# Optimization experiments

Measured on AMD Instinct MI355X. Metric: run time of the kernel, lower is better.

## Reference

```python
import jax, jax.numpy as jnp
import numpy as np

N = 100000       # nodes
E = 3200000      # edges (avg degree 32)
IN_FEATS = 128
HIDDEN = 32
PROP_STEP = 8
USE_RELU = False  # args.relu default


def setup_inputs() -> dict:
    key = jax.random.key(0)
    k1, k2, k3, k4, k5 = jax.random.split(key, 5)
    in_feat = jax.random.normal(k1, (N, IN_FEATS), jnp.float32)
    src = jax.random.randint(k2, (E,), 0, N)
    dst = jax.random.randint(k3, (E,), 0, N)
    # Glorot-ish uniform init like DGL GraphConv weights
    s1 = float(np.sqrt(6.0 / (IN_FEATS + HIDDEN)))
    s2 = float(np.sqrt(6.0 / (HIDDEN + HIDDEN)))
    W1 = jax.random.uniform(k4, (IN_FEATS, HIDDEN), jnp.float32, -s1, s1)
    b1 = jnp.zeros((HIDDEN,), jnp.float32)
    W2 = jax.random.uniform(k5, (HIDDEN, HIDDEN), jnp.float32, -s2, s2)
    b2 = jnp.zeros((HIDDEN,), jnp.float32)
    return {"in_feat": in_feat, "W1": W1, "b1": b1, "W2": W2, "b2": b2,
            "src": src, "dst": dst}


def _graph_conv(x, W, b, src, dst, out_norm, in_norm, weight_first):
    # DGL GraphConv, norm='both':
    #   h = x * out_deg^{-1/2}; (optionally h @ W); SpMM aggregate src->dst;
    #   rst = agg * in_deg^{-1/2}; (optionally @ W); + bias
    h = x * out_norm[:, None]
    if weight_first:
        h = h @ W  # [N, out]
    agg = jax.ops.segment_sum(h[src], dst, num_segments=x.shape[0])
    rst = agg * in_norm[:, None]
    if not weight_first:
        rst = rst @ W
    return rst + b


def reference(in_feat, W1, b1, W2, b2, src, dst):
    n = in_feat.shape[0]
    ones = jnp.ones((src.shape[0],), in_feat.dtype)
    out_deg = jax.ops.segment_sum(ones, src, num_segments=n)
    in_deg = jax.ops.segment_sum(ones, dst, num_segments=n)
    out_norm = jax.lax.rsqrt(jnp.maximum(out_deg, 1.0))
    in_norm = jax.lax.rsqrt(jnp.maximum(in_deg, 1.0))
    # conv1: in_feats(128) > out_feats(32) -> weight applied before aggregation
    h = _graph_conv(in_feat, W1, b1, src, dst, out_norm, in_norm, weight_first=True)
    for _ in range(1, PROP_STEP):
        if USE_RELU:
            h = jax.nn.relu(h)
        h = _graph_conv(h, W2, b2, src, dst, out_norm, in_norm, weight_first=False)
    return h
```

## Files before the change

kernel.cpp:

```cpp
#include <hip/hip_runtime.h>
#include <hip/hip_bf16.h>

#define NNODES 100000
#define NEDGES 3200000
#define INF 128
#define HID 32
#define NB 392
#define BSHIFT 8
#define NPB 256
#define BATCH 16384
#define PART_BLOCKS ((NEDGES + BATCH - 1) / BATCH)

typedef unsigned short u16;

__device__ __forceinline__ float blo(unsigned x) { return __uint_as_float(x << 16); }
__device__ __forceinline__ float bhi(unsigned x) { return __uint_as_float(x & 0xffff0000u); }
__device__ __forceinline__ u16 f2b(float f) {
    __hip_bfloat16 h = __float2bfloat16(f);
    return *reinterpret_cast<u16*>(&h);
}

__global__ void k_cnt(const int* __restrict__ src, const int* __restrict__ dst,
                      int* __restrict__ bcnt_src, int* __restrict__ bcnt_dst) {
    __shared__ int hs[NB], hd[NB];
    int tid = threadIdx.x;
    for (int i = tid; i < NB; i += 1024) { hs[i] = 0; hd[i] = 0; }
    __syncthreads();
    int start = blockIdx.x * BATCH;
    int end = start + BATCH; if (end > NEDGES) end = NEDGES;
    for (int i = start + tid; i < end; i += 1024) {
        atomicAdd(&hs[src[i] >> BSHIFT], 1);
        atomicAdd(&hd[dst[i] >> BSHIFT], 1);
    }
    __syncthreads();
    for (int i = tid; i < NB; i += 1024) {
        if (hs[i]) atomicAdd(&bcnt_src[i], hs[i]);
        if (hd[i]) atomicAdd(&bcnt_dst[i], hd[i]);
    }
}

__global__ void k_bscan(const int* __restrict__ bcnt_src, const int* __restrict__ bcnt_dst,
                        int* __restrict__ bbase_src, int* __restrict__ bbase_dst,
                        int* __restrict__ gcur_src, int* __restrict__ gcur_dst) {
    __shared__ int s[512], t[512];
    int tid = threadIdx.x;
    int vs = (tid < NB) ? bcnt_src[tid] : 0;
    int vd = (tid < NB) ? bcnt_dst[tid] : 0;
    s[tid] = vs; t[tid] = vd;
    __syncthreads();
    for (int off = 1; off < 512; off <<= 1) {
        int a = (tid >= off) ? s[tid - off] : 0;
        int b = (tid >= off) ? t[tid - off] : 0;
        __syncthreads();
        s[tid] += a; t[tid] += b;
        __syncthreads();
    }
    if (tid < NB) {
        bbase_src[tid] = s[tid] - vs;  gcur_src[tid] = s[tid] - vs;
        bbase_dst[tid] = t[tid] - vd;  gcur_dst[tid] = t[tid] - vd;
    }
}

__global__ void k_bucket2(const int* __restrict__ src, const int* __restrict__ dst,
                          int* __restrict__ gcur_src, int* __restrict__ gcur_dst,
                          int2* __restrict__ pairbuf, int* __restrict__ srctmp) {
    __shared__ int cs[NB], cd[NB];
    int tid = threadIdx.x;
    for (int i = tid; i < NB; i += 1024) { cs[i] = 0; cd[i] = 0; }
    __syncthreads();
    int start = blockIdx.x * BATCH;
    int end = start + BATCH; if (end > NEDGES) end = NEDGES;
    for (int i = start + tid; i < end; i += 1024) {
        atomicAdd(&cs[src[i] >> BSHIFT], 1);
        atomicAdd(&cd[dst[i] >> BSHIFT], 1);
    }
    __syncthreads();
    for (int i = tid; i < NB; i += 1024) {
        int c = cs[i];
        cs[i] = c ? atomicAdd(&gcur_src[i], c) : 0;
        c = cd[i];
        cd[i] = c ? atomicAdd(&gcur_dst[i], c) : 0;
    }
    __syncthreads();
    for (int i = start + tid; i < end; i += 1024) {
        int d = dst[i], s = src[i];
        int pd = atomicAdd(&cd[d >> BSHIFT], 1);
        int2 e; e.x = d; e.y = s;
        pairbuf[pd] = e;
        int ps = atomicAdd(&cs[s >> BSHIFT], 1);
        srctmp[ps] = s;
    }
}

__global__ void k_nodes(const int* __restrict__ srctmp, const int2* __restrict__ pairbuf,
                        const int* __restrict__ bbase_src, const int* __restrict__ bcnt_src,
                        const int* __restrict__ bbase_dst, const int* __restrict__ bcnt_dst,
                        float* __restrict__ out_norm, float* __restrict__ in_norm,
                        int* __restrict__ indeg, int* __restrict__ rowstart) {
    __shared__ int cnt[NPB];
    __shared__ int ss[NPB];
    int tid = threadIdx.x;
    int b = blockIdx.x;
    int srcphase = (b < NB);
    int bb = srcphase ? b : b - NB;
    int node0 = bb * NPB;
    cnt[tid] = 0;
    __syncthreads();
    if (srcphase) {
        int s0 = bbase_src[bb], n = bcnt_src[bb];
        for (int i = tid; i < n; i += 256)
            atomicAdd(&cnt[srctmp[s0 + i] - node0], 1);
        __syncthreads();
        int nn = node0 + tid;
        if (nn < NNODES) {
            int c = cnt[tid];
            out_norm[nn] = rsqrtf((float)(c > 1 ? c : 1));
        }
    } else {
        int d0 = bbase_dst[bb], n = bcnt_dst[bb];
        for (int i = tid; i < n; i += 256)
            atomicAdd(&cnt[pairbuf[d0 + i].x - node0], 1);
        __syncthreads();
        int c = cnt[tid];
        ss[tid] = c;
        __syncthreads();
        for (int off = 1; off < 256; off <<= 1) {
            int t = (tid >= off) ? ss[tid - off] : 0;
            __syncthreads();
            ss[tid] += t;
            __syncthreads();
        }
        int excl = ss[tid] - c;
        int nn = node0 + tid;
        if (nn < NNODES) {
            indeg[nn] = c;
            in_norm[nn] = rsqrtf((float)(c > 1 ? c : 1));
            rowstart[nn] = d0 + excl;
        }
    }
}

__global__ void k_place(const int2* __restrict__ pairbuf, const int* __restrict__ rowstart,
                        int* __restrict__ col) {
    __shared__ int cur[NPB];
    int tid = threadIdx.x;
    int bucket = blockIdx.x;
    int node0 = bucket * NPB;
    if (node0 >= NNODES) return;
    int n = node0 + tid;
    cur[tid] = (n < NNODES) ? rowstart[n] : 0;
    __syncthreads();
    int pstart = rowstart[node0];
    int pend   = (node0 + NPB >= NNODES) ? NEDGES : rowstart[node0 + NPB];
    for (int i = pstart + tid; i < pend; i += 256) {
        int2 e = pairbuf[i];
        int pos = atomicAdd(&cur[e.x - node0], 1);
        col[pos] = e.y;
    }
}

__global__ void k_gemm1(const float* __restrict__ x, const float* __restrict__ W1,
                        const float* __restrict__ out_norm, u16* __restrict__ t) {
    __shared__ float wlds[INF * HID];
    __shared__ float xlds[8][INF];
    int tid = threadIdx.x;
    for (int i = tid; i < INF * HID; i += 256) wlds[i] = W1[i];
    int group = tid >> 5, lane = tid & 31;
    int row = blockIdx.x * 8 + group;
    float4 xv = ((const float4*)(x + (size_t)row * INF))[lane];
    ((float4*)xlds[group])[lane] = xv;
    __syncthreads();
    float acc = 0.f;
#pragma unroll
    for (int k = 0; k < INF; ++k)
        acc += xlds[group][k] * wlds[k * HID + lane];
    t[(size_t)row * HID + lane] = f2b(acc * out_norm[row]);
}

template<int APPLY_W, int FINAL>
__global__ void k_spmm(const u16* __restrict__ gin, const int* __restrict__ rowstart,
                       const int* __restrict__ indeg, const int* __restrict__ col,
                       const float* __restrict__ in_norm, const float* __restrict__ out_norm,
                       const float* __restrict__ W, const float* __restrict__ bias,
                       void* __restrict__ gout) {
    __shared__ float wlds[HID * HID];
    __shared__ float sh[8][HID];
    int tid = threadIdx.x, lane = tid & 31, group = tid >> 5;
    int g = lane >> 2, f = lane & 3;
    if (APPLY_W) {
        for (int i = tid; i < HID * HID; i += 256) wlds[i] = W[i];
        __syncthreads();
    }
    int n = blockIdx.x * 8 + group;
    int start = rowstart[n];
    int deg   = indeg[n];
    const uint4* gin16 = (const uint4*)gin;

    float a[8];
#pragma unroll
    for (int j = 0; j < 8; ++j) a[j] = 0.f;

    int base = 0;
    for (; base + 32 <= deg; base += 32) {
        int c = col[start + base + lane];
#pragma unroll
        for (int t = 0; t < 4; ++t) {
            int s = __shfl(c, t * 8 + g, 32);
            uint4 v = gin16[(size_t)s * 4 + f];
            a[0] += blo(v.x); a[1] += bhi(v.x);
            a[2] += blo(v.y); a[3] += bhi(v.y);
            a[4] += blo(v.z); a[5] += bhi(v.z);
            a[6] += blo(v.w); a[7] += bhi(v.w);
        }
    }
    if (base < deg) {
        int rem = deg - base;
        int c = (base + lane < deg) ? col[start + base + lane] : 0;
#pragma unroll
        for (int t = 0; t < 4; ++t) {
            if (t * 8 < rem) {
                int e = t * 8 + g;
                int s = __shfl(c, e, 32);
                uint4 v = gin16[(size_t)s * 4 + f];
                float m = (e < rem) ? 1.f : 0.f;
                a[0] = fmaf(m, blo(v.x), a[0]); a[1] = fmaf(m, bhi(v.x), a[1]);
                a[2] = fmaf(m, blo(v.y), a[2]); a[3] = fmaf(m, bhi(v.y), a[3]);
                a[4] = fmaf(m, blo(v.z), a[4]); a[5] = fmaf(m, bhi(v.z), a[5]);
                a[6] = fmaf(m, blo(v.w), a[6]); a[7] = fmaf(m, bhi(v.w), a[7]);
            }
        }
    }
#pragma unroll
    for (int j = 0; j < 8; ++j) {
        a[j] += __shfl_xor(a[j], 4, 32);
        a[j] += __shfl_xor(a[j], 8, 32);
        a[j] += __shfl_xor(a[j], 16, 32);
    }
    float inm = in_norm[n];
    if (g == 0) {
        float4 lo = make_float4(a[0] * inm, a[1] * inm, a[2] * inm, a[3] * inm);
        float4 hi = make_float4(a[4] * inm, a[5] * inm, a[6] * inm, a[7] * inm);
        *(float4*)&sh[group][f * 8]     = lo;
        *(float4*)&sh[group][f * 8 + 4] = hi;
    }
    float res;
    if (APPLY_W) {
        float o = bias[lane];
#pragma unroll
        for (int k = 0; k < HID; ++k)
            o += sh[group][k] * wlds[k * HID + lane];
        res = o;
    } else {
        res = sh[group][lane] + bias[lane];
    }
    if (FINAL) ((float*)gout)[(size_t)n * HID + lane] = res;
    else       ((u16*)gout)[(size_t)n * HID + lane] = f2b(res * out_norm[n]);
}

extern "C" void kernel_launch(void* const* d_in, const int* in_sizes, int n_in,
                              void* d_out, int out_size, void* d_ws, size_t ws_size,
                              hipStream_t stream) {
    const float* in_feat = (const float*)d_in[0];
    const float* W1      = (const float*)d_in[1];
    const float* b1      = (const float*)d_in[2];
    const float* W2      = (const float*)d_in[3];
    const float* b2      = (const float*)d_in[4];
    const int*   src     = (const int*)d_in[5];
    const int*   dst     = (const int*)d_in[6];
    float*       out     = (float*)d_out;

    const int N = NNODES, E = NEDGES;
    int* bcnt_src  = (int*)d_ws;
    int* bcnt_dst  = bcnt_src + 512;
    int* bbase_src = bcnt_dst + 512;
    int* bbase_dst = bbase_src + 512;
    int* gcur_src  = bbase_dst + 512;
    int* gcur_dst  = gcur_src + 512;
    int* indeg     = gcur_dst + 512;
    int* rowstart  = indeg + N;
    float* out_norm = (float*)(rowstart + N);
    float* in_norm  = out_norm + N;
    int*   col      = (int*)(in_norm + N);
    void*  bufreg   = (void*)(col + E);
    int2*  pairbuf  = (int2*)bufreg;
    int*   srctmp   = col;
    u16*   bufA16   = (u16*)bufreg;
    u16*   bufB16   = bufA16 + (size_t)N * HID;
    size_t need = ((size_t)3072 + 4 * N + E + (size_t)2 * N * HID) * 4;
    if (ws_size < need) return;

    hipMemsetAsync(bcnt_src, 0, 1024 * sizeof(int), stream);

    k_cnt    <<<PART_BLOCKS, 1024, 0, stream>>>(src, dst, bcnt_src, bcnt_dst);
    k_bscan  <<<1, 512, 0, stream>>>(bcnt_src, bcnt_dst, bbase_src, bbase_dst,
                                     gcur_src, gcur_dst);
    k_bucket2<<<PART_BLOCKS, 1024, 0, stream>>>(src, dst, gcur_src, gcur_dst,
                                                pairbuf, srctmp);
    k_nodes  <<<2 * NB, 256, 0, stream>>>(srctmp, pairbuf, bbase_src, bcnt_src,
                                          bbase_dst, bcnt_dst, out_norm, in_norm,
                                          indeg, rowstart);
    k_place  <<<NB, 256, 0, stream>>>(pairbuf, rowstart, col);

    k_gemm1<<<N / 8, 256, 0, stream>>>(in_feat, W1, out_norm, bufA16);

    k_spmm<0, 0><<<N / 8, 256, 0, stream>>>(bufA16, rowstart, indeg, col, in_norm,
                                            out_norm, W2, b1, bufB16);

    u16* cur = bufB16; u16* nxt = bufA16;
    for (int i = 0; i < 6; ++i) {
        k_spmm<1, 0><<<N / 8, 256, 0, stream>>>(cur, rowstart, indeg, col, in_norm,
                                                out_norm, W2, b2, nxt);
        u16* tmp = cur; cur = nxt; nxt = tmp;
    }
    k_spmm<1, 1><<<N / 8, 256, 0, stream>>>(cur, rowstart, indeg, col, in_norm,
                                            out_norm, W2, b2, out);
}
```

Before: 502.2 us.

## Stage bucketed edges in shared memory for contiguous global scatter writes

The bucketing kernel now sorts each batch of edges by bucket inside shared memory, using local ranks and a block-wide prefix scan, before writing them out. Runs of edges for the same bucket are therefore stored contiguously to pairbuf and srctmp instead of being scattered randomly to global memory. The batch size is halved so the int2 staging buffer fits in LDS. This adds scans, syncs and LDS traffic and doubles the number of partition blocks and global atomics, in exchange for better write coalescing in what is only one part of a larger pipeline.

After: 480.8 us. 1.04x faster.

```diff
diff --git a/kernel.cpp b/kernel.cpp
--- a/kernel.cpp
+++ b/kernel.cpp
@@ -8,7 +8,7 @@
 #define NB 392
 #define BSHIFT 8
 #define NPB 256
-#define BATCH 16384
+#define BATCH 8192
 #define PART_BLOCKS ((NEDGES + BATCH - 1) / BATCH)
 
 typedef unsigned short u16;
@@ -64,31 +64,87 @@
 __global__ void k_bucket2(const int* __restrict__ src, const int* __restrict__ dst,
                           int* __restrict__ gcur_src, int* __restrict__ gcur_dst,
                           int2* __restrict__ pairbuf, int* __restrict__ srctmp) {
-    __shared__ int cs[NB], cd[NB];
-    int tid = threadIdx.x;
-    for (int i = tid; i < NB; i += 1024) { cs[i] = 0; cd[i] = 0; }
-    __syncthreads();
+    __shared__ int2 stage2[BATCH];
+    __shared__ int cnt[NB], excl[NB], gbase[NB];
+    __shared__ int sc[512];
+    int* stage1 = (int*)stage2;
+    int tid = threadIdx.x;
     int start = blockIdx.x * BATCH;
     int end = start + BATCH; if (end > NEDGES) end = NEDGES;
-    for (int i = start + tid; i < end; i += 1024) {
-        atomicAdd(&cs[src[i] >> BSHIFT], 1);
-        atomicAdd(&cd[dst[i] >> BSHIFT], 1);
-    }
-    __syncthreads();
-    for (int i = tid; i < NB; i += 1024) {
-        int c = cs[i];
-        cs[i] = c ? atomicAdd(&gcur_src[i], c) : 0;
-        c = cd[i];
-        cd[i] = c ? atomicAdd(&gcur_dst[i], c) : 0;
-    }
-    __syncthreads();
-    for (int i = start + tid; i < end; i += 1024) {
-        int d = dst[i], s = src[i];
-        int pd = atomicAdd(&cd[d >> BSHIFT], 1);
-        int2 e; e.x = d; e.y = s;
-        pairbuf[pd] = e;
-        int ps = atomicAdd(&cs[s >> BSHIFT], 1);
-        srctmp[ps] = s;
+    int cntE = end - start;
+
+    int dd[8], sv[8], rk[8];
+
+    for (int i = tid; i < NB; i += 1024) cnt[i] = 0;
+    __syncthreads();
+#pragma unroll
+    for (int k = 0; k < 8; ++k) {
+        int i = start + tid + k * 1024;
+        dd[k] = -1;
+        if (i < end) {
+            dd[k] = dst[i]; sv[k] = src[i];
+            rk[k] = atomicAdd(&cnt[dd[k] >> BSHIFT], 1);
+        }
+    }
+    __syncthreads();
+    if (tid < 512) sc[tid] = (tid < NB) ? cnt[tid] : 0;
+    __syncthreads();
+    for (int off = 1; off < 512; off <<= 1) {
+        int v = (tid < 512 && tid >= off) ? sc[tid - off] : 0;
+        __syncthreads();
+        if (tid < 512) sc[tid] += v;
+        __syncthreads();
+    }
+    if (tid < NB) {
+        excl[tid] = sc[tid] - cnt[tid];
+        int c = cnt[tid];
+        gbase[tid] = c ? atomicAdd(&gcur_dst[tid], c) : 0;
+    }
+    __syncthreads();
+#pragma unroll
+    for (int k = 0; k < 8; ++k)
+        if (dd[k] >= 0) {
+            int2 e; e.x = dd[k]; e.y = sv[k];
+            stage2[excl[dd[k] >> BSHIFT] + rk[k]] = e;
+        }
+    __syncthreads();
+    for (int j = tid; j < cntE; j += 1024) {
+        int2 e = stage2[j];
+        int b = e.x >> BSHIFT;
+        pairbuf[gbase[b] + (j - excl[b])] = e;
+    }
+    __syncthreads();
+
+    for (int i = tid; i < NB; i += 1024) cnt[i] = 0;
+    __syncthreads();
+#pragma unroll
+    for (int k = 0; k < 8; ++k)
+        if (dd[k] >= 0)
+            rk[k] = atomicAdd(&cnt[sv[k] >> BSHIFT], 1);
+    __syncthreads();
+    if (tid < 512) sc[tid] = (tid < NB) ? cnt[tid] : 0;
+    __syncthreads();
+    for (int off = 1; off < 512; off <<= 1) {
+        int v = (tid < 512 && tid >= off) ? sc[tid - off] : 0;
+        __syncthreads();
+        if (tid < 512) sc[tid] += v;
+        __syncthreads();
+    }
+    if (tid < NB) {
+        excl[tid] = sc[tid] - cnt[tid];
+        int c = cnt[tid];
+        gbase[tid] = c ? atomicAdd(&gcur_src[tid], c) : 0;
+    }
+    __syncthreads();
+#pragma unroll
+    for (int k = 0; k < 8; ++k)
+        if (dd[k] >= 0)
+            stage1[excl[sv[k] >> BSHIFT] + rk[k]] = sv[k];
+    __syncthreads();
+    for (int j = tid; j < cntE; j += 1024) {
+        int v = stage1[j];
+        int b = v >> BSHIFT;
+        srctmp[gbase[b] + (j - excl[b])] = v;
     }
 }
 
```
